# Kernel optimization log

Measured on AMD Instinct MI355X. Metric: run time of the kernel, lower is better.

The kernel has to match this reference:

```python
import jax, jax.numpy as jnp
import numpy as np

STRIDES = (8, 16, 32, 64, 128)
SCORE_THR = 0.05
IOU_THR = 0.6
MAX_NUM = 150
USE_CTR = True
B, NC = 64, 20
HW = (128, 64, 32, 16, 8)


def _reshape(feat):
    # [B,C,H,W] -> [B,H*W,C]
    b, c, h, w = feat.shape
    return feat.transpose(0, 2, 3, 1).reshape(b, h * w, c)


def _decode(feat, stride):
    # feat: [B,4,H,W] reg offsets; returns [B,HW,4] boxes (x1,y1,x2,y2)
    _, _, h, w = feat.shape
    xs = jnp.arange(w, dtype=jnp.float32) * stride + (stride // 2)
    ys = jnp.arange(h, dtype=jnp.float32) * stride + (stride // 2)
    yy, xx = jnp.meshgrid(ys, xs, indexing='ij')
    coords = jnp.stack([xx.reshape(-1), yy.reshape(-1)], axis=-1)  # [HW,2]
    off = _reshape(feat) * stride  # [B,HW,4]
    xy1 = coords[None] - off[..., :2]
    xy2 = coords[None] + off[..., 2:]
    return jnp.concatenate([xy1, xy2], axis=-1)


def _nms_single(scores, ids, boxes, valid):
    # scores already sorted descending (from top_k); class-aware offset NMS.
    coord_max = jnp.max(jnp.where(valid[:, None], boxes, -jnp.inf))
    coord_max = jnp.where(jnp.isfinite(coord_max), coord_max, 0.0)
    ob = boxes + (ids.astype(boxes.dtype) * (coord_max + 1.0))[:, None]
    x1, y1, x2, y2 = ob[:, 0], ob[:, 1], ob[:, 2], ob[:, 3]
    areas = (x2 - x1 + 1.0) * (y2 - y1 + 1.0)
    xmin = jnp.maximum(x1[:, None], x1[None, :])
    ymin = jnp.maximum(y1[:, None], y1[None, :])
    xmax = jnp.minimum(x2[:, None], x2[None, :])
    ymax = jnp.minimum(y2[:, None], y2[None, :])
    ow = jnp.clip(xmax - xmin, 0.0)
    oh = jnp.clip(ymax - ymin, 0.0)
    overlap = ow * oh
    union = jnp.clip(areas[:, None] + areas[None, :] - overlap, 1e-10)
    iou = overlap / union  # [N,N]
    n = scores.shape[0]
    idx = jnp.arange(n)

    def body(i, keep):
        sup = keep[i] & (iou[i] > IOU_THR) & (idx > i)
        return keep & ~sup

    return jax.lax.fori_loop(0, n, body, valid)


def setup_inputs() -> dict:
    key = jax.random.key(0)
    ks = jax.random.split(key, 15)
    out = {}
    for li, hw in enumerate(HW):
        out[f'cls{li}'] = jax.random.normal(ks[li], (B, NC, hw, hw), jnp.float32)
        out[f'reg{li}'] = jax.random.uniform(ks[5 + li], (B, 4, hw, hw), jnp.float32)
        out[f'ctr{li}'] = jax.random.normal(ks[10 + li], (B, 1, hw, hw), jnp.float32)
    return out


def reference(cls0, cls1, cls2, cls3, cls4,
              reg0, reg1, reg2, reg3, reg4,
              ctr0, ctr1, ctr2, ctr3, ctr4):
    cls_feats = (cls0, cls1, cls2, cls3, cls4)
    reg_feats = (reg0, reg1, reg2, reg3, reg4)
    ctr_feats = (ctr0, ctr1, ctr2, ctr3, ctr4)

    cls_logits = jnp.concatenate([_reshape(f) for f in cls_feats], axis=1)  # [B,A,NC]
    ctr_logits = jnp.concatenate([_reshape(f) for f in ctr_feats], axis=1)  # [B,A,1]
    cls_preds = jax.nn.sigmoid(cls_logits)
    ctr_preds = jax.nn.sigmoid(ctr_logits)

    cls_scores = jnp.max(cls_preds, axis=-1)  # [B,A]
    cls_ids = jnp.argmax(cls_preds, axis=-1) + 1  # [B,A]
    if USE_CTR:
        cls_scores = jnp.sqrt(cls_scores * ctr_preds[..., 0])

    boxes = jnp.concatenate(
        [_decode(f, s) for f, s in zip(reg_feats, STRIDES)], axis=1)  # [B,A,4]

    top_scores, top_idx = jax.lax.top_k(cls_scores, MAX_NUM)  # sorted desc
    top_ids = jnp.take_along_axis(cls_ids, top_idx, axis=1)
    top_boxes = jnp.take_along_axis(boxes, top_idx[..., None], axis=1)

    valid = top_scores > SCORE_THR
    keep = jax.vmap(_nms_single)(top_scores, top_ids, top_boxes, valid)

    out_scores = jnp.where(keep, top_scores, 0.0)
    out_ids = jnp.where(keep, top_ids, 0)
    out_boxes = jnp.where(keep[..., None], top_boxes, 0.0)
    return out_scores, out_ids, out_boxes, keep
```

## Files before the change

### kernel.cpp

```cpp
#include <hip/hip_runtime.h>
#include <cstdint>
#include <cstddef>

#define NPTS 21824
#define NB   64
#define NCLS 20
#define MAXN 150
#define NCHUNK 11
#define CHSZ 2048

typedef unsigned long long u64;
typedef unsigned int u32;


template<int T>
__device__ __forceinline__ void bitonic2048_desc(u64* keys)
{
    const int tid = threadIdx.x;
    for (int k = 2; k <= 2048; k <<= 1) {
        for (int j = k >> 1; j > 0; j >>= 1) {
            __syncthreads();
            #pragma unroll
            for (int t = tid; t < 1024; t += T) {
                int i = ((t & ~(j - 1)) << 1) | (t & (j - 1));
                int pr = i | j;
                u64 a = keys[i], c = keys[pr];
                bool desc = ((i & k) == 0);
                if (desc ? (a < c) : (a > c)) { keys[i] = c; keys[pr] = a; }
            }
        }
    }
    __syncthreads();
}

__global__ __launch_bounds__(512) void k_part(
    const float* __restrict__ c0, const float* __restrict__ c1,
    const float* __restrict__ c2, const float* __restrict__ c3,
    const float* __restrict__ c4,
    const float* __restrict__ t0, const float* __restrict__ t1,
    const float* __restrict__ t2, const float* __restrict__ t3,
    const float* __restrict__ t4,
    u64* __restrict__ cand)
{
    __shared__ u64 keys[CHSZ];
    const int tid   = threadIdx.x;
    const int chunk = blockIdx.x;
    const int b     = blockIdx.y;

    const int pl = tid * 4;
    const int p  = chunk * CHSZ + pl;
    u64 kk0 = 0, kk1 = 0, kk2 = 0, kk3 = 0;
    if (p < NPTS) {
        const float* cp; const float* tp; int base; size_t hw;
        if (p < 16384)      { cp = c0; tp = t0; base = 0;     hw = 16384; }
        else if (p < 20480) { cp = c1; tp = t1; base = 16384; hw = 4096;  }
        else if (p < 21504) { cp = c2; tp = t2; base = 20480; hw = 1024;  }
        else if (p < 21760) { cp = c3; tp = t3; base = 21504; hw = 256;   }
        else                { cp = c4; tp = t4; base = 21760; hw = 64;    }
        int q = p - base;
        const float* cb = cp + (size_t)b * NCLS * hw + q;

        float u0 = INFINITY, u1 = INFINITY, u2 = INFINITY, u3 = INFINITY;
        for (int c = 0; c < NCLS; ++c) {
            const float4 v = *reinterpret_cast<const float4*>(cb + (size_t)c * hw);
            u0 = fminf(u0, expf(-v.x));
            u1 = fminf(u1, expf(-v.y));
            u2 = fminf(u2, expf(-v.z));
            u3 = fminf(u3, expf(-v.w));
        }
        const float4 cv = *reinterpret_cast<const float4*>(tp + (size_t)b * hw + q);
        float best, sct, sc;
        best = 1.0f / (1.0f + u0); sct = 1.0f / (1.0f + expf(-cv.x));
        sc = sqrtf(__fmul_rn(best, sct));
        kk0 = ((u64)__float_as_uint(sc) << 32) | (u32)(21823 - p);
        best = 1.0f / (1.0f + u1); sct = 1.0f / (1.0f + expf(-cv.y));
        sc = sqrtf(__fmul_rn(best, sct));
        kk1 = ((u64)__float_as_uint(sc) << 32) | (u32)(21823 - (p + 1));
        best = 1.0f / (1.0f + u2); sct = 1.0f / (1.0f + expf(-cv.z));
        sc = sqrtf(__fmul_rn(best, sct));
        kk2 = ((u64)__float_as_uint(sc) << 32) | (u32)(21823 - (p + 2));
        best = 1.0f / (1.0f + u3); sct = 1.0f / (1.0f + expf(-cv.w));
        sc = sqrtf(__fmul_rn(best, sct));
        kk3 = ((u64)__float_as_uint(sc) << 32) | (u32)(21823 - (p + 3));
    }
    keys[pl + 0] = kk0; keys[pl + 1] = kk1;
    keys[pl + 2] = kk2; keys[pl + 3] = kk3;

    bitonic2048_desc<512>(keys);

    if (tid < MAXN)
        cand[((size_t)b * NCHUNK + chunk) * MAXN + tid] = keys[tid];
}

__global__ __launch_bounds__(1024) void k_final(
    const float* __restrict__ c0, const float* __restrict__ c1,
    const float* __restrict__ c2, const float* __restrict__ c3,
    const float* __restrict__ c4,
    const float* __restrict__ r0, const float* __restrict__ r1,
    const float* __restrict__ r2, const float* __restrict__ r3,
    const float* __restrict__ r4,
    const u64* __restrict__ cand,
    float* __restrict__ out)
{
    const int NC2 = NCHUNK * MAXN;
    __shared__ u64 keys[CHSZ];
    __shared__ float bx0[MAXN], bx1[MAXN], bx2[MAXN], bx3[MAXN];
    __shared__ float ox1[MAXN], oy1[MAXN], ox2[MAXN], oy2[MAXN], area[MAXN];
    __shared__ float sc[MAXN];
    __shared__ int   idv[MAXN];
    __shared__ u64 sup[MAXN][3];
    __shared__ u64 keepw[3];
    __shared__ float shcmax;
    __shared__ float wmax[16];

    const int b = blockIdx.x, tid = threadIdx.x;

    for (int i = tid; i < CHSZ; i += 1024)
        keys[i] = (i < NC2) ? cand[(size_t)b * NC2 + i] : 0ull;

    bitonic2048_desc<1024>(keys);

    if (tid < MAXN) {
        u64 key = keys[tid];
        sc[tid] = __uint_as_float((u32)(key >> 32));
        int p   = 21823 - (int)(key & 0x7FFFu);

        const float* rp; const float* cp; int base, dim, lg, st;
        if (p < 16384)      { rp = r0; cp = c0; base = 0;     dim = 128; lg = 7; st = 8;   }
        else if (p < 20480) { rp = r1; cp = c1; base = 16384; dim = 64;  lg = 6; st = 16;  }
        else if (p < 21504) { rp = r2; cp = c2; base = 20480; dim = 32;  lg = 5; st = 32;  }
        else if (p < 21760) { rp = r3; cp = c3; base = 21504; dim = 16;  lg = 4; st = 64;  }
        else                { rp = r4; cp = c4; base = 21760; dim = 8;   lg = 3; st = 128; }

        int q = p - base;
        size_t hw = (size_t)dim * dim;

        const float* cb = cp + (size_t)b * NCLS * hw + q;
        float best = -1.0f; int bi = 0;
        for (int c = 0; c < NCLS; ++c) {
            float v  = cb[(size_t)c * hw];
            float sg = 1.0f / (1.0f + expf(-v));
            if (sg > best) { best = sg; bi = c; }
        }
        idv[tid] = bi + 1;

        int y = q >> lg;
        int x = q & (dim - 1);
        float s  = (float)st;
        float cx = (float)(x * st + (st >> 1));
        float cy = (float)(y * st + (st >> 1));
        const float* rg = rp + (size_t)b * 4 * hw + q;
        float a0 = rg[0], a1 = rg[hw], a2 = rg[2 * hw], a3 = rg[3 * hw];
        bx0[tid] = __fsub_rn(cx, __fmul_rn(a0, s));
        bx1[tid] = __fsub_rn(cy, __fmul_rn(a1, s));
        bx2[tid] = __fadd_rn(cx, __fmul_rn(a2, s));
        bx3[tid] = __fadd_rn(cy, __fmul_rn(a3, s));
    }
    __syncthreads();

    float m = -INFINITY;
    if (tid < MAXN && sc[tid] > 0.05f)
        m = fmaxf(fmaxf(bx0[tid], bx1[tid]), fmaxf(bx2[tid], bx3[tid]));
    #pragma unroll
    for (int off = 32; off >= 1; off >>= 1) m = fmaxf(m, __shfl_xor(m, off));
    if ((tid & 63) == 0) wmax[tid >> 6] = m;
    if (tid < 192) {
        bool val = (tid < MAXN) && (sc[tid] > 0.05f);
        u64 mask = __ballot(val);
        if ((tid & 63) == 0) keepw[tid >> 6] = mask;
    }
    __syncthreads();
    if (tid == 0) {
        float mm = -INFINITY;
        for (int w = 0; w < 16; ++w) mm = fmaxf(mm, wmax[w]);
        shcmax = isfinite(mm) ? mm : 0.0f;
    }
    __syncthreads();

    float cm1 = __fadd_rn(shcmax, 1.0f);
    if (tid < MAXN) {
        float off = __fmul_rn((float)idv[tid], cm1);
        float X1 = __fadd_rn(bx0[tid], off);
        float Y1 = __fadd_rn(bx1[tid], off);
        float X2 = __fadd_rn(bx2[tid], off);
        float Y2 = __fadd_rn(bx3[tid], off);
        ox1[tid] = X1; oy1[tid] = Y1; ox2[tid] = X2; oy2[tid] = Y2;
        area[tid] = __fmul_rn(__fadd_rn(__fsub_rn(X2, X1), 1.0f),
                              __fadd_rn(__fsub_rn(Y2, Y1), 1.0f));
    }
    __syncthreads();

    if (tid < MAXN * 3) {
        int i = tid / 3;
        int w = tid - i * 3;
        float x1i = ox1[i], y1i = oy1[i], x2i = ox2[i], y2i = oy2[i], ai = area[i];
        u64 bits = 0ull;
        for (int e = 0; e < 64; ++e) {
            int j = w * 64 + e;
            if (j >= MAXN) break;
            float xmin = fmaxf(x1i, ox1[j]);
            float ymin = fmaxf(y1i, oy1[j]);
            float xmax = fminf(x2i, ox2[j]);
            float ymax = fminf(y2i, oy2[j]);
            float ow = fmaxf(__fsub_rn(xmax, xmin), 0.0f);
            float oh = fmaxf(__fsub_rn(ymax, ymin), 0.0f);
            float ov = __fmul_rn(ow, oh);
            float un = fmaxf(__fsub_rn(__fadd_rn(ai, area[j]), ov), 1e-10f);
            float iou = __fdiv_rn(ov, un);
            if (iou > 0.6f) bits |= (1ull << e);
        }
        sup[i][w] = bits;
    }
    __syncthreads();

    if (tid < 64) {
        const int l = tid;
        u64 kw   = (l < 3) ? keepw[l]  : 0ull;
        u64 scur = (l < 3) ? sup[0][l] : 0ull;
        for (int i = 0; i < MAXN; ++i) {
            u64 snext = (l < 3 && i + 1 < MAXN) ? sup[i + 1][l] : 0ull;
            u64 kwwi = __shfl(kw, i >> 6);
            if ((kwwi >> (i & 63)) & 1ull) {
                int lo = l * 64;
                u64 allow;
                if (i < lo)            allow = ~0ull;
                else if (i - lo >= 63) allow = 0ull;
                else                   allow = ~((1ull << (i - lo + 1)) - 1ull);
                kw &= ~(scur & allow);
            }
            scur = snext;
        }
        if (l < 3) keepw[l] = kw;
    }
    __syncthreads();

    if (tid < MAXN) {
        bool kp = (keepw[tid >> 6] >> (tid & 63)) & 1ull;
        int o = b * MAXN + tid;
        float* oSc = out;
        float* oId = out + NB * MAXN;
        float* oBx = out + 2 * NB * MAXN;
        float* oKp = out + 2 * NB * MAXN + NB * MAXN * 4;
        oSc[o] = kp ? sc[tid] : 0.0f;
        oId[o] = kp ? (float)idv[tid] : 0.0f;
        oBx[o * 4 + 0] = kp ? bx0[tid] : 0.0f;
        oBx[o * 4 + 1] = kp ? bx1[tid] : 0.0f;
        oBx[o * 4 + 2] = kp ? bx2[tid] : 0.0f;
        oBx[o * 4 + 3] = kp ? bx3[tid] : 0.0f;
        oKp[o] = kp ? 1.0f : 0.0f;
    }
}

extern "C" void kernel_launch(void* const* d_in, const int* in_sizes, int n_in,
                              void* d_out, int out_size, void* d_ws, size_t ws_size,
                              hipStream_t stream)
{
    const float* cls[5]; const float* reg[5]; const float* ctr[5];
    for (int li = 0; li < 5; ++li) {
        cls[li] = (const float*)d_in[3 * li + 0];
        reg[li] = (const float*)d_in[3 * li + 1];
        ctr[li] = (const float*)d_in[3 * li + 2];
    }

    u64* cand = (u64*)d_ws;

    dim3 g1(NCHUNK, NB);
    k_part<<<g1, 512, 0, stream>>>(cls[0], cls[1], cls[2], cls[3], cls[4],
                                   ctr[0], ctr[1], ctr[2], ctr[3], ctr[4],
                                   cand);
    k_final<<<NB, 1024, 0, stream>>>(cls[0], cls[1], cls[2], cls[3], cls[4],
                                     reg[0], reg[1], reg[2], reg[3], reg[4],
                                     cand, (float*)d_out);
}
```

Measured before the change: 270.9 us.

## Replace bitonic sorts with radix-bisection threshold selection and rank sort

Both kernels drop the full 2048-element bitonic sort and instead find a key threshold by bisecting bits with block-wide counts. Keys at or above the threshold are compacted with a shared atomic into up to 186 slots, and the final kernel ranks the survivors by counting to place the top 150. The partial kernel also takes the max of the raw logits before applying the sigmoid, so it computes one exp per point instead of twenty, and it processes 8 points per thread with 256-thread blocks. The aim is to cut sort barriers and transcendental work. The risk is that ties or truncation at the cap could select different candidates when many keys share high bits.

```diff
diff --git a/kernel.cpp b/kernel.cpp
--- a/kernel.cpp
+++ b/kernel.cpp
@@ -8,32 +8,39 @@
 #define MAXN 150
 #define NCHUNK 11
 #define CHSZ 2048
+#define CAP  186
 
 typedef unsigned long long u64;
 typedef unsigned int u32;
 
 
-template<int T>
-__device__ __forceinline__ void bitonic2048_desc(u64* keys)
+__device__ __forceinline__ u64 bisect_threshold(const u64 (&key)[8], int total,
+                                                int (*wcnt)[4], int cap)
 {
-    const int tid = threadIdx.x;
-    for (int k = 2; k <= 2048; k <<= 1) {
-        for (int j = k >> 1; j > 0; j >>= 1) {
-            __syncthreads();
-            #pragma unroll
-            for (int t = tid; t < 1024; t += T) {
-                int i = ((t & ~(j - 1)) << 1) | (t & (j - 1));
-                int pr = i | j;
-                u64 a = keys[i], c = keys[pr];
-                bool desc = ((i & k) == 0);
-                if (desc ? (a < c) : (a > c)) { keys[i] = c; keys[pr] = a; }
-            }
-        }
-    }
-    __syncthreads();
+    const int tid  = threadIdx.x;
+    const int lane = tid & 63, wv = tid >> 6;
+    u64 T = 0;
+    int count = total;
+    int it = 0;
+    for (int bbit = 62; bbit >= 0; --bbit) {
+        if (bbit == 31) bbit = 14;
+        if (count <= cap) break;
+        u64 Tt = T | (1ull << bbit);
+        int c = 0;
+        #pragma unroll
+        for (int i = 0; i < 8; ++i) c += (key[i] >= Tt) ? 1 : 0;
+        for (int off = 32; off; off >>= 1) c += __shfl_xor(c, off);
+        if (lane == 0) wcnt[it & 1][wv] = c;
+        __syncthreads();
+        int tot = wcnt[it & 1][0] + wcnt[it & 1][1]
+                + wcnt[it & 1][2] + wcnt[it & 1][3];
+        if (tot >= MAXN) { T = Tt; count = tot; }
+        ++it;
+    }
+    return T;
 }
 
-__global__ __launch_bounds__(512) void k_part(
+__global__ __launch_bounds__(256) void k_part(
     const float* __restrict__ c0, const float* __restrict__ c1,
     const float* __restrict__ c2, const float* __restrict__ c3,
     const float* __restrict__ c4,
@@ -42,57 +49,71 @@
     const float* __restrict__ t4,
     u64* __restrict__ cand)
 {
-    __shared__ u64 keys[CHSZ];
+    __shared__ int wcnt[2][4];
+    __shared__ int cnt;
     const int tid   = threadIdx.x;
     const int chunk = blockIdx.x;
     const int b     = blockIdx.y;
-
-    const int pl = tid * 4;
-    const int p  = chunk * CHSZ + pl;
-    u64 kk0 = 0, kk1 = 0, kk2 = 0, kk3 = 0;
-    if (p < NPTS) {
+    const int pl    = tid * 8;
+    const int p0    = chunk * CHSZ + pl;
+
+    u64 key[8];
+    #pragma unroll
+    for (int i = 0; i < 8; ++i) key[i] = 0;
+
+    if (p0 < NPTS) {
         const float* cp; const float* tp; int base; size_t hw;
-        if (p < 16384)      { cp = c0; tp = t0; base = 0;     hw = 16384; }
-        else if (p < 20480) { cp = c1; tp = t1; base = 16384; hw = 4096;  }
-        else if (p < 21504) { cp = c2; tp = t2; base = 20480; hw = 1024;  }
-        else if (p < 21760) { cp = c3; tp = t3; base = 21504; hw = 256;   }
-        else                { cp = c4; tp = t4; base = 21760; hw = 64;    }
-        int q = p - base;
+        if (p0 < 16384)      { cp = c0; tp = t0; base = 0;     hw = 16384; }
+        else if (p0 < 20480) { cp = c1; tp = t1; base = 16384; hw = 4096;  }
+        else if (p0 < 21504) { cp = c2; tp = t2; base = 20480; hw = 1024;  }
+        else if (p0 < 21760) { cp = c3; tp = t3; base = 21504; hw = 256;   }
+        else                 { cp = c4; tp = t4; base = 21760; hw = 64;    }
+        int q = p0 - base;
         const float* cb = cp + (size_t)b * NCLS * hw + q;
 
-        float u0 = INFINITY, u1 = INFINITY, u2 = INFINITY, u3 = INFINITY;
-        for (int c = 0; c < NCLS; ++c) {
-            const float4 v = *reinterpret_cast<const float4*>(cb + (size_t)c * hw);
-            u0 = fminf(u0, expf(-v.x));
-            u1 = fminf(u1, expf(-v.y));
-            u2 = fminf(u2, expf(-v.z));
-            u3 = fminf(u3, expf(-v.w));
-        }
-        const float4 cv = *reinterpret_cast<const float4*>(tp + (size_t)b * hw + q);
-        float best, sct, sc;
-        best = 1.0f / (1.0f + u0); sct = 1.0f / (1.0f + expf(-cv.x));
-        sc = sqrtf(__fmul_rn(best, sct));
-        kk0 = ((u64)__float_as_uint(sc) << 32) | (u32)(21823 - p);
-        best = 1.0f / (1.0f + u1); sct = 1.0f / (1.0f + expf(-cv.y));
-        sc = sqrtf(__fmul_rn(best, sct));
-        kk1 = ((u64)__float_as_uint(sc) << 32) | (u32)(21823 - (p + 1));
-        best = 1.0f / (1.0f + u2); sct = 1.0f / (1.0f + expf(-cv.z));
-        sc = sqrtf(__fmul_rn(best, sct));
-        kk2 = ((u64)__float_as_uint(sc) << 32) | (u32)(21823 - (p + 2));
-        best = 1.0f / (1.0f + u3); sct = 1.0f / (1.0f + expf(-cv.w));
-        sc = sqrtf(__fmul_rn(best, sct));
-        kk3 = ((u64)__float_as_uint(sc) << 32) | (u32)(21823 - (p + 3));
-    }
-    keys[pl + 0] = kk0; keys[pl + 1] = kk1;
-    keys[pl + 2] = kk2; keys[pl + 3] = kk3;
-
-    bitonic2048_desc<512>(keys);
-
-    if (tid < MAXN)
-        cand[((size_t)b * NCHUNK + chunk) * MAXN + tid] = keys[tid];
+        float4 m0 = *reinterpret_cast<const float4*>(cb);
+        float4 m1 = *reinterpret_cast<const float4*>(cb + 4);
+        for (int c = 1; c < NCLS; ++c) {
+            float4 v0 = *reinterpret_cast<const float4*>(cb + (size_t)c * hw);
+            float4 v1 = *reinterpret_cast<const float4*>(cb + (size_t)c * hw + 4);
+            m0.x = fmaxf(m0.x, v0.x); m0.y = fmaxf(m0.y, v0.y);
+            m0.z = fmaxf(m0.z, v0.z); m0.w = fmaxf(m0.w, v0.w);
+            m1.x = fmaxf(m1.x, v1.x); m1.y = fmaxf(m1.y, v1.y);
+            m1.z = fmaxf(m1.z, v1.z); m1.w = fmaxf(m1.w, v1.w);
+        }
+        const float* tb = tp + (size_t)b * hw + q;
+        float4 q0 = *reinterpret_cast<const float4*>(tb);
+        float4 q1 = *reinterpret_cast<const float4*>(tb + 4);
+
+        float mm[8] = {m0.x, m0.y, m0.z, m0.w, m1.x, m1.y, m1.z, m1.w};
+        float cc[8] = {q0.x, q0.y, q0.z, q0.w, q1.x, q1.y, q1.z, q1.w};
+        #pragma unroll
+        for (int i = 0; i < 8; ++i) {
+            float best = 1.0f / (1.0f + expf(-mm[i]));
+            float sct  = 1.0f / (1.0f + expf(-cc[i]));
+            float sc   = sqrtf(__fmul_rn(best, sct));
+            key[i] = ((u64)__float_as_uint(sc) << 32)
+                   | (u32)(21823 - (p0 + i));
+        }
+    }
+
+    u64 T = bisect_threshold(key, CHSZ, wcnt, CAP);
+
+    if (tid == 0) cnt = 0;
+    __syncthreads();
+    u64* outp = cand + ((size_t)b * NCHUNK + chunk) * CAP;
+    #pragma unroll
+    for (int i = 0; i < 8; ++i) {
+        if (key[i] >= T) {
+            int pos = atomicAdd(&cnt, 1);
+            if (pos < CAP) outp[pos] = key[i];
+        }
+    }
+    __syncthreads();
+    for (int i = cnt + tid; i < CAP; i += 256) outp[i] = 0;
 }
 
-__global__ __launch_bounds__(1024) void k_final(
+__global__ __launch_bounds__(256) void k_final(
     const float* __restrict__ c0, const float* __restrict__ c1,
     const float* __restrict__ c2, const float* __restrict__ c3,
     const float* __restrict__ c4,
@@ -102,8 +123,11 @@
     const u64* __restrict__ cand,
     float* __restrict__ out)
 {
-    const int NC2 = NCHUNK * MAXN;
-    __shared__ u64 keys[CHSZ];
+    const int NC2 = NCHUNK * CAP;
+    __shared__ int wcnt[2][4];
+    __shared__ int cnt;
+    __shared__ u64 win[CAP];
+    __shared__ u64 srt[MAXN];
     __shared__ float bx0[MAXN], bx1[MAXN], bx2[MAXN], bx3[MAXN];
     __shared__ float ox1[MAXN], oy1[MAXN], ox2[MAXN], oy2[MAXN], area[MAXN];
     __shared__ float sc[MAXN];
@@ -111,19 +135,42 @@
     __shared__ u64 sup[MAXN][3];
     __shared__ u64 keepw[3];
     __shared__ float shcmax;
-    __shared__ float wmax[16];
+    __shared__ float wmax[4];
 
     const int b = blockIdx.x, tid = threadIdx.x;
 
-    for (int i = tid; i < CHSZ; i += 1024)
-        keys[i] = (i < NC2) ? cand[(size_t)b * NC2 + i] : 0ull;
-
-    bitonic2048_desc<1024>(keys);
+    u64 key[8];
+    #pragma unroll
+    for (int j = 0; j < 8; ++j) {
+        int i = j * 256 + tid;
+        key[j] = (i < NC2) ? cand[(size_t)b * NC2 + i] : 0ull;
+    }
+
+    u64 T = bisect_threshold(key, CHSZ, wcnt, CAP);
+
+    if (tid == 0) cnt = 0;
+    if (tid < MAXN) srt[tid] = 0ull;
+    __syncthreads();
+    #pragma unroll
+    for (int j = 0; j < 8; ++j) {
+        if (key[j] >= T) {
+            int pos = atomicAdd(&cnt, 1);
+            if (pos < CAP) win[pos] = key[j];
+        }
+    }
+    __syncthreads();
+    int C = min(cnt, CAP);
+    if (tid < C) {
+        u64 mk = win[tid]; int r = 0;
+        for (int j = 0; j < C; ++j) r += (win[j] > mk) ? 1 : 0;
+        if (r < MAXN) srt[r] = mk;
+    }
+    __syncthreads();
 
     if (tid < MAXN) {
-        u64 key = keys[tid];
-        sc[tid] = __uint_as_float((u32)(key >> 32));
-        int p   = 21823 - (int)(key & 0x7FFFu);
+        u64 kk = srt[tid];
+        sc[tid] = __uint_as_float((u32)(kk >> 32));
+        int p   = 21823 - (int)(kk & 0x7FFFu);
 
         const float* rp; const float* cp; int base, dim, lg, st;
         if (p < 16384)      { rp = r0; cp = c0; base = 0;     dim = 128; lg = 7; st = 8;   }
@@ -171,8 +218,7 @@
     }
     __syncthreads();
     if (tid == 0) {
-        float mm = -INFINITY;
-        for (int w = 0; w < 16; ++w) mm = fmaxf(mm, wmax[w]);
+        float mm = fmaxf(fmaxf(wmax[0], wmax[1]), fmaxf(wmax[2], wmax[3]));
         shcmax = isfinite(mm) ? mm : 0.0f;
     }
     __syncthreads();
@@ -190,9 +236,9 @@
     }
     __syncthreads();
 
-    if (tid < MAXN * 3) {
-        int i = tid / 3;
-        int w = tid - i * 3;
+    for (int t = tid; t < MAXN * 3; t += 256) {
+        int i = t / 3;
+        int w = t - i * 3;
         float x1i = ox1[i], y1i = oy1[i], x2i = ox2[i], y2i = oy2[i], ai = area[i];
         u64 bits = 0ull;
         for (int e = 0; e < 64; ++e) {
@@ -265,10 +311,10 @@
     u64* cand = (u64*)d_ws;
 
     dim3 g1(NCHUNK, NB);
-    k_part<<<g1, 512, 0, stream>>>(cls[0], cls[1], cls[2], cls[3], cls[4],
+    k_part<<<g1, 256, 0, stream>>>(cls[0], cls[1], cls[2], cls[3], cls[4],
                                    ctr[0], ctr[1], ctr[2], ctr[3], ctr[4],
                                    cand);
-    k_final<<<NB, 1024, 0, stream>>>(cls[0], cls[1], cls[2], cls[3], cls[4],
-                                     reg[0], reg[1], reg[2], reg[3], reg[4],
-                                     cand, (float*)d_out);
+    k_final<<<NB, 256, 0, stream>>>(cls[0], cls[1], cls[2], cls[3], cls[4],
+                                    reg[0], reg[1], reg[2], reg[3], reg[4],
+                                    cand, (float*)d_out);
 }
```

After: 254.2 us. 1.07x faster.
